# Performance work log

Hardware: AMD Instinct MI355X
Metric: run time of the kernel (lower is better)

The kernel has to match this reference:

```python
import jax, jax.numpy as jnp
import numpy as np

# Regular batched tree: BS roots, arity A, depth D (root=level 0, leaves=level D)
BS, A, D = 32, 4, 6
V, E, H = 50000, 256, 256
LEVEL_SIZES = [BS * A ** d for d in range(D + 1)]
OFFSETS = np.concatenate([[0], np.cumsum(LEVEL_SIZES)]).astype(np.int64)
TOTAL = int(OFFSETS[-1])  # 174752


def gru_cell(x, h, w_ih, w_hh, b_ih, b_hh):
    # torch nn.GRU single step, gate order (r, z, n)
    gi = x @ w_ih.T + b_ih
    gh = h @ w_hh.T + b_hh
    ir, iz, inn = jnp.split(gi, 3, axis=-1)
    hr, hz, hn = jnp.split(gh, 3, axis=-1)
    r = jax.nn.sigmoid(ir + hr)
    z = jax.nn.sigmoid(iz + hz)
    n = jnp.tanh(inn + r * hn)
    return (1.0 - z) * n + z * h


def child_attention(h_last, sent_weight, sent_bias, context_weight):
    # Reproduces hidden_per_child stacking: ch[g,c,i,:] = h_last[g,c] if c==i else 0.
    G, S, _ = h_last.shape
    eye = jnp.eye(S, dtype=h_last.dtype)
    ch = h_last[:, :, None, :] * eye[None, :, :, None]          # [G,S(c),S(i),H]
    t1 = jnp.tanh(jnp.einsum('gcih,hk->gcik', ch, sent_weight) + sent_bias[0])
    u = jnp.tanh(jnp.einsum('gcik,ko->gci', t1, context_weight))  # [G,S,S]
    w = jax.nn.softmax(u, axis=1)                                # softmax over c (the P axis)
    return jnp.einsum('gci,gcih->gih', w, ch)                    # [G,S,H]


def setup_inputs() -> dict:
    key = jax.random.key(0)
    ks = jax.random.split(key, 9)
    s = 1.0 / np.sqrt(H)
    return {
        'tokens': jax.random.randint(ks[0], (TOTAL,), 0, V, dtype=jnp.int32),
        'embedding': jax.random.normal(ks[1], (V, E), jnp.float32) * 0.1,
        'w_ih': jax.random.uniform(ks[2], (3 * H, E), jnp.float32, -s, s),
        'w_hh': jax.random.uniform(ks[3], (3 * H, H), jnp.float32, -s, s),
        'b_ih': jax.random.uniform(ks[4], (3 * H,), jnp.float32, -s, s),
        'b_hh': jax.random.uniform(ks[5], (3 * H,), jnp.float32, -s, s),
        'sent_weight': jax.random.normal(ks[6], (H, H), jnp.float32) * 0.05,
        'sent_bias': jax.random.normal(ks[7], (1, H), jnp.float32) * 0.05,
        'context_weight': jax.random.normal(ks[8], (H, 1), jnp.float32) * 0.05,
    }


def reference(tokens, embedding, w_ih, w_hh, b_ih, b_hh, sent_weight, sent_bias, context_weight):
    def tok(d):
        return tokens[int(OFFSETS[d]):int(OFFSETS[d + 1])]

    gru = lambda x, h: gru_cell(x, h, w_ih, w_hh, b_ih, b_hh)

    # leaves: no children -> zero initial hidden
    h_levels = {D: gru(embedding[tok(D)], jnp.zeros((LEVEL_SIZES[D], H), jnp.float32))}

    for d in range(D - 1, -1, -1):
        h_child = h_levels[d + 1].reshape(-1, A, H)   # [N_d, A, H]
        # duplicate index_copy in torch: only last child's hidden survives per parent
        h_last = h_child[:, A - 1, :]                 # [N_d, H]
        S = BS if d == 0 else A                       # call size: bs at root, A siblings otherwise
        groups = h_last.reshape(-1, S, H)
        chs = child_attention(groups, sent_weight, sent_bias, context_weight).reshape(-1, H)
        h_levels[d] = gru(embedding[tok(d)], chs)

    # final max over node_list: root entry has all bs rows; every other call's entry has
    # only row b = hn of the LAST sibling (duplicate valid_indices), zeros elsewhere.
    out = jnp.maximum(jnp.zeros((BS, H), jnp.float32), h_levels[0])
    for d in range(1, D + 1):
        last_sib = h_levels[d].reshape(BS, -1, A, H)[:, :, A - 1, :].max(axis=1)
        out = jnp.maximum(out, last_sib)
    return out
```

## Files before the change

kernel.cpp:

```cpp
#include <hip/hip_runtime.h>
#include <hip/hip_bf16.h>
#include <math.h>


typedef unsigned short u16;
typedef unsigned int u32;
typedef __attribute__((ext_vector_type(8))) short s8;
typedef __attribute__((ext_vector_type(4))) float f4;
#define MFMA16(a, b, c) __builtin_amdgcn_mfma_f32_16x16x32_bf16(a, b, c, 0, 0, 0)

__device__ __forceinline__ u16 f2bf(float f) {
  u32 x = __float_as_uint(f);
  return (u16)((x + 0x7fffu + ((x >> 16) & 1u)) >> 16);
}
__device__ __forceinline__ float bf2f(u16 u) { return __uint_as_float(((u32)u) << 16); }
__device__ __forceinline__ float sigmoidf_(float x) {
  return __builtin_amdgcn_rcpf(1.f + __builtin_amdgcn_exp2f(-1.4426950408889634f * x));
}
__device__ __forceinline__ float tanhf_(float x) {
  x = fminf(fmaxf(x, -15.f), 15.f);
  float t = __builtin_amdgcn_exp2f(-2.8853900817779268f * x);
  return 1.f - 2.f * t * __builtin_amdgcn_rcpf(1.f + t);
}
__device__ __forceinline__ void gload_lds16(const void* g, void* l) {
  typedef const __attribute__((address_space(1))) unsigned int* gp_t;
  typedef __attribute__((address_space(3))) unsigned int* lp_t;
  __builtin_amdgcn_global_load_lds((gp_t)g, (lp_t)l, 16, 0, 0);
}
__device__ __forceinline__ void stage_row(const float* __restrict__ emb, int tok,
                                          u16* aX, int r, int lane) {
  float4 v = ((const float4*)(emb + (size_t)tok * 256))[lane];
  uint2 val = {(u32)f2bf(v.x) | ((u32)f2bf(v.y) << 16),
               (u32)f2bf(v.z) | ((u32)f2bf(v.w) << 16)};
  *(uint2*)&aX[r * 256 + ((((lane >> 1)) ^ (r & 7)) << 3) + (lane & 1) * 4] = val;
}

__global__ void prep_pack(const float* __restrict__ wih, const float* __restrict__ whh,
                          const float* __restrict__ sw, const float* __restrict__ sb,
                          const float* __restrict__ cw,
                          u16* __restrict__ wihP, u16* __restrict__ whhPh,
                          u16* __restrict__ whhPl, u16* __restrict__ swPh,
                          float* __restrict__ u0p, int* __restrict__ outI) {
  int b = blockIdx.x, t = threadIdx.x;
  if (b == 320) {
    #pragma unroll
    for (int k = 0; k < 32; ++k) outI[k * 256 + t] = 0;
    if (t < 64) {
      float s = 0.f;
      #pragma unroll
      for (int q = 0; q < 4; ++q) { int k = t + 64 * q; s += tanhf(sb[k]) * cw[k]; }
      #pragma unroll
      for (int off = 32; off >= 1; off >>= 1) s += __shfl_xor(s, off);
      if (t == 0) u0p[0] = tanhf(s);
    }
    return;
  }
  int g = b * 256 + t;
  const float* src;
  u16* dst;
  int idx, NF, lomode, trans;
  if (g < 24576)      { idx = g;         src = wih; dst = wihP;  NF = 48; lomode = 0; trans = 1; }
  else if (g < 49152) { idx = g - 24576; src = whh; dst = whhPh; NF = 48; lomode = 0; trans = 1; }
  else if (g < 73728) { idx = g - 49152; src = whh; dst = whhPl; NF = 48; lomode = 1; trans = 1; }
  else                { idx = g - 73728; src = sw;  dst = swPh;  NF = 16; lomode = 0; trans = 0; }
  int lane = idx & 63;
  int t2 = idx >> 6;
  int nf = t2 % NF, kb = t2 / NF;
  int n = nf * 16 + (lane & 15);
  int k0 = kb * 32 + (lane >> 4) * 8;
  float v[8];
  if (trans) {
    const float4* p = (const float4*)(src + (size_t)n * 256 + k0);
    float4 a = p[0], b2 = p[1];
    v[0] = a.x; v[1] = a.y; v[2] = a.z; v[3] = a.w;
    v[4] = b2.x; v[5] = b2.y; v[6] = b2.z; v[7] = b2.w;
  } else {
    #pragma unroll
    for (int j = 0; j < 8; ++j) v[j] = src[(size_t)(k0 + j) * 256 + n];
  }
  u16 o[8];
  #pragma unroll
  for (int j = 0; j < 8; ++j) {
    u16 hi = f2bf(v[j]);
    o[j] = lomode ? f2bf(v[j] - bf2f(hi)) : hi;
  }
  u32* d = (u32*)(dst + (size_t)idx * 8);
  #pragma unroll
  for (int j = 0; j < 4; ++j) d[j] = (u32)o[2 * j] | ((u32)o[2 * j + 1] << 16);
}

__global__ __launch_bounds__(512, 2)
void levelAB_kernel(const int* __restrict__ t6, const int* __restrict__ t5,
                    const float* __restrict__ emb,
                    const u16* __restrict__ wihP, const u16* __restrict__ whhPh,
                    const u16* __restrict__ whhPl, const u16* __restrict__ swPh,
                    const float* __restrict__ bih, const float* __restrict__ bhh,
                    const float* __restrict__ sb, const float* __restrict__ cw,
                    const float* __restrict__ u0p,
                    u16* __restrict__ Hs5Hi, u16* __restrict__ Hs5Lo,
                    int* __restrict__ outI) {
  __shared__ u16 aX6[32768];
  __shared__ u16 aX5[8192];
  __shared__ u16 aH[2][8192];
  __shared__ float pm[8][32];
  __shared__ float scl[32];

  const int t = threadIdx.x;
  const int rb = blockIdx.x;
  const int lane = t & 63, w = t >> 6;
  const int asub = lane >> 4, l15 = lane & 15;
  const float LN3 = 1.0986122886681098f;

  {
    #pragma unroll
    for (int rr = 0; rr < 16; ++rr) {
      int r = 16 * w + rr;
      int tok = t6[4 * (128 * rb + r) + 3];
      stage_row(emb, tok, aX6, r, lane);
    }
    #pragma unroll
    for (int rr = 0; rr < 4; ++rr) {
      int r = 4 * w + rr;
      int tok = t5[4 * (32 * rb + r) + 3];
      stage_row(emb, tok, aX5, r, lane);
    }
  }
  __syncthreads();

  #pragma unroll 1
  for (int pass = 0; pass < 4; ++pass) {
    const int sp = pass >> 1, jc = pass & 1;
    const int cfx = 2 * w + jc;
    f4 gi[3][4];
    #pragma unroll
    for (int g = 0; g < 3; ++g)
      #pragma unroll
      for (int mf = 0; mf < 4; ++mf) gi[g][mf] = (f4){0.f, 0.f, 0.f, 0.f};
    s8 bw[2][3];
    auto LB = [&](int kb, int pb) {
      #pragma unroll
      for (int g = 0; g < 3; ++g)
        bw[pb][g] = *(const s8*)&wihP[((size_t)(kb * 48 + 16 * g + cfx) * 64 + lane) * 8];
    };
    LB(0, 0);
    #pragma unroll
    for (int kb = 0; kb < 8; ++kb) {
      const int pb = kb & 1;
      if (kb < 7) LB(kb + 1, pb ^ 1);
      s8 axh[4];
      #pragma unroll
      for (int mf = 0; mf < 4; ++mf) {
        int abase = (64 * sp + 16 * mf + l15) * 256 + (((kb * 4 + asub) ^ (l15 & 7)) << 3);
        axh[mf] = *(const s8*)&aX6[abase];
      }
      #pragma unroll
      for (int g = 0; g < 3; ++g)
        #pragma unroll
        for (int mf = 0; mf < 4; ++mf)
          gi[g][mf] = MFMA16(axh[mf], bw[pb][g], gi[g][mf]);
    }
    const int col = 16 * cfx + l15;
    const float bi0 = bih[col], bi1 = bih[256 + col], bi2 = bih[512 + col];
    const float bh0 = bhh[col], bh1 = bhh[256 + col], bh2 = bhh[512 + col];
    float cm = -1e30f;
    #pragma unroll
    for (int mf = 0; mf < 4; ++mf) {
      #pragma unroll
      for (int j = 0; j < 4; ++j) {
        float r = sigmoidf_(gi[0][mf][j] + bi0 + bh0);
        float z = sigmoidf_(gi[1][mf][j] + bi1 + bh1);
        float n = tanhf_(gi[2][mf][j] + bi2 + r * bh2);
        float h = (1.f - z) * n;
        if (j == 3) {
          int ci = 16 * sp + 4 * mf + asub;
          u16 hi = f2bf(h);
          u16 lo = f2bf(h - bf2f(hi));
          int hidx = ((col >> 3) * 32 + ci) * 8 + (col & 7);
          aH[0][hidx] = hi;
          aH[1][hidx] = lo;
        }
        cm = fmaxf(cm, h);
      }
    }
    cm = fmaxf(cm, __shfl_xor(cm, 16));
    cm = fmaxf(cm, __shfl_xor(cm, 32));
    if (asub == 0)
      atomicMax(outI + (size_t)(rb >> 3) * 256 + col, __float_as_int(cm));
  }
  __syncthreads();

  f4 sa[2][2];
  #pragma unroll
  for (int jc = 0; jc < 2; ++jc)
    #pragma unroll
    for (int mf = 0; mf < 2; ++mf) sa[jc][mf] = (f4){0.f, 0.f, 0.f, 0.f};
  {
    s8 bsw[2][2];
    auto LSW = [&](int kb, int pb) {
      #pragma unroll
      for (int jc = 0; jc < 2; ++jc)
        bsw[pb][jc] = *(const s8*)&swPh[((size_t)(kb * 16 + 2 * w + jc) * 64 + lane) * 8];
    };
    LSW(0, 0);
    #pragma unroll
    for (int kb = 0; kb < 8; ++kb) {
      const int pb = kb & 1;
      if (kb < 7) LSW(kb + 1, pb ^ 1);
      s8 ahh[2], ahl[2];
      #pragma unroll
      for (int mf = 0; mf < 2; ++mf) {
        int abase = ((kb * 4 + asub) * 32 + 16 * mf + l15) * 8;
        ahh[mf] = *(const s8*)&aH[0][abase];
        ahl[mf] = *(const s8*)&aH[1][abase];
      }
      #pragma unroll
      for (int jc = 0; jc < 2; ++jc) {
        sa[jc][0] = MFMA16(ahh[0], bsw[pb][jc], sa[jc][0]);
        sa[jc][1] = MFMA16(ahh[1], bsw[pb][jc], sa[jc][1]);
        sa[jc][0] = MFMA16(ahl[0], bsw[pb][jc], sa[jc][0]);
        sa[jc][1] = MFMA16(ahl[1], bsw[pb][jc], sa[jc][1]);
      }
    }
  }
  {
    float part[2][4] = {{0.f, 0.f, 0.f, 0.f}, {0.f, 0.f, 0.f, 0.f}};
    #pragma unroll
    for (int jc = 0; jc < 2; ++jc) {
      int k = 16 * (2 * w + jc) + l15;
      float sbk = sb[k], cwk = cw[k];
      #pragma unroll
      for (int mf = 0; mf < 2; ++mf)
        #pragma unroll
        for (int j = 0; j < 4; ++j) part[mf][j] += tanhf_(sa[jc][mf][j] + sbk) * cwk;
    }
    #pragma unroll
    for (int mf = 0; mf < 2; ++mf)
      #pragma unroll
      for (int j = 0; j < 4; ++j) {
        part[mf][j] += __shfl_xor(part[mf][j], 1);
        part[mf][j] += __shfl_xor(part[mf][j], 2);
        part[mf][j] += __shfl_xor(part[mf][j], 4);
        part[mf][j] += __shfl_xor(part[mf][j], 8);
      }
    if (l15 == 0) {
      #pragma unroll
      for (int mf = 0; mf < 2; ++mf)
        #pragma unroll
        for (int j = 0; j < 4; ++j) pm[w][16 * mf + 4 * asub + j] = part[mf][j];
    }
    __syncthreads();
    if (t < 32) {
      float v = 0.f;
      #pragma unroll
      for (int q = 0; q < 8; ++q) v += pm[q][t];
      scl[t] = sigmoidf_(tanhf_(v) - u0p[0] - LN3);
    }
    __syncthreads();
  }
  #pragma unroll 1
  for (int pass = 0; pass < 4; ++pass) {
    const int p = pass >> 1, mf = pass & 1;
    const int cf = w + 8 * p;
    f4 gi5[3], gh5[3];
    #pragma unroll
    for (int g = 0; g < 3; ++g) {
      gi5[g] = (f4){0.f, 0.f, 0.f, 0.f};
      gh5[g] = (f4){0.f, 0.f, 0.f, 0.f};
    }
    #pragma unroll
    for (int kb = 0; kb < 8; ++kb) {
      s8 bwi[3], bwh[3], bwl[3];
      #pragma unroll
      for (int g = 0; g < 3; ++g) {
        size_t bo = ((size_t)(kb * 48 + 16 * g + cf) * 64 + lane) * 8;
        bwi[g] = *(const s8*)&wihP[bo];
        bwh[g] = *(const s8*)&whhPh[bo];
        bwl[g] = *(const s8*)&whhPl[bo];
      }
      int axb = (16 * mf + l15) * 256 + (((kb * 4 + asub) ^ (l15 & 7)) << 3);
      s8 axh = *(const s8*)&aX5[axb];
      int abase = ((kb * 4 + asub) * 32 + 16 * mf + l15) * 8;
      s8 ahh = *(const s8*)&aH[0][abase];
      s8 ahl = *(const s8*)&aH[1][abase];
      #pragma unroll
      for (int g = 0; g < 3; ++g) {
        gi5[g] = MFMA16(axh, bwi[g], gi5[g]);
        gh5[g] = MFMA16(ahh, bwh[g], gh5[g]);
        gh5[g] = MFMA16(ahl, bwh[g], gh5[g]);
        gh5[g] = MFMA16(ahh, bwl[g], gh5[g]);
      }
    }
    const int col = 16 * cf + l15;
    const float bi0 = bih[col], bi1 = bih[256 + col], bi2 = bih[512 + col];
    const float bh0 = bhh[col], bh1 = bhh[256 + col], bh2 = bhh[512 + col];
    const int r0 = 16 * mf + 4 * asub;
    float cm = -1e30f;
    #pragma unroll
    for (int j = 0; j < 4; ++j) {
      const int row = r0 + j;
      const int i = 32 * rb + row;
      float sc = scl[row];
      float ir = gi5[0][j] + bi0;
      float iz = gi5[1][j] + bi1;
      float inn = gi5[2][j] + bi2;
      float g0 = bh0 + sc * gh5[0][j];
      float g1 = bh1 + sc * gh5[1][j];
      float g2 = bh2 + sc * gh5[2][j];
      int hidx = ((col >> 3) * 32 + row) * 8 + (col & 7);
      float hp = sc * (bf2f(aH[0][hidx]) + bf2f(aH[1][hidx]));
      float r = sigmoidf_(ir + g0);
      float z = sigmoidf_(iz + g1);
      float n = tanhf_(inn + r * g2);
      float h = (1.f - z) * n + z * hp;
      if (j == 3) {
        u16 hi = f2bf(h);
        u16 lo = f2bf(h - bf2f(hi));
        Hs5Hi[(size_t)(i >> 2) * 256 + col] = hi;
        Hs5Lo[(size_t)(i >> 2) * 256 + col] = lo;
      }
      cm = fmaxf(cm, h);
    }
    cm = fmaxf(cm, __shfl_xor(cm, 16));
    cm = fmaxf(cm, __shfl_xor(cm, 32));
    if (asub == 0)
      atomicMax(outI + (size_t)(rb >> 3) * 256 + col, __float_as_int(cm));
  }
}

__global__ __launch_bounds__(512, 2)
void levelB_kernel(const int* __restrict__ tokens, const float* __restrict__ emb,
                   const u16* __restrict__ wihP, const u16* __restrict__ whhPh,
                   const u16* __restrict__ whhPl, const u16* __restrict__ swPh,
                   const float* __restrict__ bih, const float* __restrict__ bhh,
                   const float* __restrict__ sb, const float* __restrict__ cw,
                   const float* __restrict__ u0p,
                   const u16* __restrict__ HpHi, const u16* __restrict__ HpLo,
                   u16* __restrict__ HoutHi, u16* __restrict__ HoutLo,
                   int* __restrict__ outI, float logSm1, int bshift) {
  __shared__ u16 aX[8192];
  __shared__ u16 aH[2][8192];
  __shared__ float pm[8][32];
  __shared__ float scl[32];

  const int t = threadIdx.x;
  const int rb = blockIdx.x >> 1, cb = blockIdx.x & 1;
  const int i0 = rb * 32;
  const int lane = t & 63, w = t >> 6;

  {
    int row = lane & 31;
    const u16* sh = HpHi + ((size_t)(i0 + row) << 8);
    const u16* sl = HpLo + ((size_t)(i0 + row) << 8);
    #pragma unroll
    for (int c = 0; c < 2; ++c) {
      int cg = w * 4 + c * 2 + (lane >> 5);
      int lb = w * 1024 + c * 512;
      gload_lds16(sh + (cg << 3), &aH[0][lb]);
      gload_lds16(sl + (cg << 3), &aH[1][lb]);
    }
  }
  {
    #pragma unroll
    for (int rr = 0; rr < 4; ++rr) {
      int r = 4 * w + rr;
      int tok = tokens[4 * (i0 + r) + 3];
      stage_row(emb, tok, aX, r, lane);
    }
  }
  __syncthreads();

  const int asub = lane >> 4, l15 = lane & 15;
  const int cfg = 8 * cb + w;

  f4 gi[3][2], gh[3][2], sa[2][2];
  #pragma unroll
  for (int g = 0; g < 3; ++g)
    #pragma unroll
    for (int mf = 0; mf < 2; ++mf) {
      gi[g][mf] = (f4){0.f, 0.f, 0.f, 0.f};
      gh[g][mf] = (f4){0.f, 0.f, 0.f, 0.f};
    }
  #pragma unroll
  for (int jc = 0; jc < 2; ++jc)
    #pragma unroll
    for (int mf = 0; mf < 2; ++mf) sa[jc][mf] = (f4){0.f, 0.f, 0.f, 0.f};

  #pragma unroll
  for (int kb = 0; kb < 8; ++kb) {
    s8 bwi[3], bwh[3], bwl[3], bsw[2];
    #pragma unroll
    for (int g = 0; g < 3; ++g) {
      size_t bo = ((size_t)(kb * 48 + 16 * g + cfg) * 64 + lane) * 8;
      bwi[g] = *(const s8*)&wihP[bo];
      bwh[g] = *(const s8*)&whhPh[bo];
      bwl[g] = *(const s8*)&whhPl[bo];
    }
    #pragma unroll
    for (int jc = 0; jc < 2; ++jc) {
      size_t so = ((size_t)(kb * 16 + 2 * w + jc) * 64 + lane) * 8;
      bsw[jc] = *(const s8*)&swPh[so];
    }
    s8 axh[2], ahh[2], ahl[2];
    #pragma unroll
    for (int mf = 0; mf < 2; ++mf) {
      int axb = (16 * mf + l15) * 256 + (((kb * 4 + asub) ^ (l15 & 7)) << 3);
      axh[mf] = *(const s8*)&aX[axb];
      int abase = ((kb * 4 + asub) * 32 + 16 * mf + l15) * 8;
      ahh[mf] = *(const s8*)&aH[0][abase];
      ahl[mf] = *(const s8*)&aH[1][abase];
    }
    #pragma unroll
    for (int g = 0; g < 3; ++g) {
      gi[g][0] = MFMA16(axh[0], bwi[g], gi[g][0]);
      gi[g][1] = MFMA16(axh[1], bwi[g], gi[g][1]);
      gh[g][0] = MFMA16(ahh[0], bwh[g], gh[g][0]);
      gh[g][1] = MFMA16(ahh[1], bwh[g], gh[g][1]);
      gh[g][0] = MFMA16(ahl[0], bwh[g], gh[g][0]);
      gh[g][1] = MFMA16(ahl[1], bwh[g], gh[g][1]);
      gh[g][0] = MFMA16(ahh[0], bwl[g], gh[g][0]);
      gh[g][1] = MFMA16(ahh[1], bwl[g], gh[g][1]);
    }
    #pragma unroll
    for (int jc = 0; jc < 2; ++jc) {
      sa[jc][0] = MFMA16(ahh[0], bsw[jc], sa[jc][0]);
      sa[jc][1] = MFMA16(ahh[1], bsw[jc], sa[jc][1]);
      sa[jc][0] = MFMA16(ahl[0], bsw[jc], sa[jc][0]);
      sa[jc][1] = MFMA16(ahl[1], bsw[jc], sa[jc][1]);
    }
  }

  {
    float part[2][4] = {{0.f, 0.f, 0.f, 0.f}, {0.f, 0.f, 0.f, 0.f}};
    #pragma unroll
    for (int jc = 0; jc < 2; ++jc) {
      int k = 16 * (2 * w + jc) + l15;
      float sbk = sb[k], cwk = cw[k];
      #pragma unroll
      for (int mf = 0; mf < 2; ++mf)
        #pragma unroll
        for (int j = 0; j < 4; ++j) part[mf][j] += tanhf_(sa[jc][mf][j] + sbk) * cwk;
    }
    #pragma unroll
    for (int mf = 0; mf < 2; ++mf)
      #pragma unroll
      for (int j = 0; j < 4; ++j) {
        part[mf][j] += __shfl_xor(part[mf][j], 1);
        part[mf][j] += __shfl_xor(part[mf][j], 2);
        part[mf][j] += __shfl_xor(part[mf][j], 4);
        part[mf][j] += __shfl_xor(part[mf][j], 8);
      }
    if (l15 == 0) {
      #pragma unroll
      for (int mf = 0; mf < 2; ++mf)
        #pragma unroll
        for (int j = 0; j < 4; ++j) pm[w][16 * mf + 4 * asub + j] = part[mf][j];
    }
    __syncthreads();
    if (t < 32) {
      float v = 0.f;
      #pragma unroll
      for (int q = 0; q < 8; ++q) v += pm[q][t];
      scl[t] = sigmoidf_(tanhf_(v) - u0p[0] - logSm1);
    }
    __syncthreads();
  }

  {
    const int col = 16 * cfg + l15;
    const float bi0 = bih[col], bi1 = bih[256 + col], bi2 = bih[512 + col];
    const float bh0 = bhh[col], bh1 = bhh[256 + col], bh2 = bhh[512 + col];
    float cmax = -1e30f;
    #pragma unroll
    for (int mf = 0; mf < 2; ++mf) {
      const int r0 = 16 * mf + 4 * asub;
      #pragma unroll
      for (int j = 0; j < 4; ++j) {
        const int row = r0 + j;
        const int i = i0 + row;
        float sc = scl[row];
        float ir = gi[0][mf][j] + bi0;
        float iz = gi[1][mf][j] + bi1;
        float inn = gi[2][mf][j] + bi2;
        float g0 = bh0 + sc * gh[0][mf][j];
        float g1 = bh1 + sc * gh[1][mf][j];
        float g2 = bh2 + sc * gh[2][mf][j];
        int hidx = ((col >> 3) * 32 + row) * 8 + (col & 7);
        float hp = sc * (bf2f(aH[0][hidx]) + bf2f(aH[1][hidx]));
        float r = sigmoidf_(ir + g0);
        float z = sigmoidf_(iz + g1);
        float n = tanhf_(inn + r * g2);
        float h = (1.f - z) * n + z * hp;
        if ((i & 3) == 3) {
          u16 hi = f2bf(h);
          u16 lo = f2bf(h - bf2f(hi));
          HoutHi[(size_t)(i >> 2) * 256 + col] = hi;
          HoutLo[(size_t)(i >> 2) * 256 + col] = lo;
        }
        cmax = fmaxf(cmax, h);
      }
    }
    cmax = fmaxf(cmax, __shfl_xor(cmax, 16));
    cmax = fmaxf(cmax, __shfl_xor(cmax, 32));
    if (asub == 0)
      atomicMax(outI + (size_t)(i0 >> bshift) * 256 + col, __float_as_int(cmax));
  }
}

struct Bregs {
  s8 wi[3], wh[3], wl[3], sw[4];
};
__device__ __forceinline__ void loadB(int kb, int cf, int wq, int lane,
                                      const u16* __restrict__ wihP,
                                      const u16* __restrict__ whhPh,
                                      const u16* __restrict__ whhPl,
                                      const u16* __restrict__ swPh, Bregs& r) {
  #pragma unroll
  for (int g = 0; g < 3; ++g) {
    size_t bo = ((size_t)(kb * 48 + 16 * g + cf) * 64 + lane) * 8;
    r.wi[g] = *(const s8*)&wihP[bo];
    r.wh[g] = *(const s8*)&whhPh[bo];
    r.wl[g] = *(const s8*)&whhPl[bo];
  }
  #pragma unroll
  for (int c = 0; c < 4; ++c) {
    size_t so = ((size_t)(kb * 16 + 4 * wq + c) * 64 + lane) * 8;
    r.sw[c] = *(const s8*)&swPh[so];
  }
}

template <bool ROOT>
__global__ __launch_bounds__(512, 2)
void tail_kernel(const int* __restrict__ tokens, const float* __restrict__ emb,
                 const u16* __restrict__ wihP, const u16* __restrict__ whhPh,
                 const u16* __restrict__ whhPl, const u16* __restrict__ swPh,
                 const float* __restrict__ bih, const float* __restrict__ bhh,
                 const float* __restrict__ sb, const float* __restrict__ cw,
                 const float* __restrict__ u0p,
                 const u16* __restrict__ HpHi, const u16* __restrict__ HpLo,
                 u16* __restrict__ HoutHi, u16* __restrict__ HoutLo,
                 int* __restrict__ outI, float logSm1, int bshift, int store_mode) {
  __shared__ u16 aX[8192];
  __shared__ u16 aH[2][8192];
  __shared__ float pm[8][32];
  __shared__ float scl[32];

  const int t = threadIdx.x;
  const int rb = blockIdx.x >> 2, cb = blockIdx.x & 3;
  const int i0 = rb * 32;
  const int lane = t & 63, w = t >> 6;

  {
    int row = lane & 31;
    const u16* sh = HpHi + ((size_t)(i0 + row) << 8);
    const u16* sl = HpLo + ((size_t)(i0 + row) << 8);
    #pragma unroll
    for (int c = 0; c < 2; ++c) {
      int cg = w * 4 + c * 2 + (lane >> 5);
      int lb = w * 1024 + c * 512;
      gload_lds16(sh + (cg << 3), &aH[0][lb]);
      gload_lds16(sl + (cg << 3), &aH[1][lb]);
    }
  }
  {
    #pragma unroll
    for (int rr = 0; rr < 4; ++rr) {
      int r = 4 * w + rr;
      int tok = tokens[ROOT ? (i0 + r) : (4 * (i0 + r) + 3)];
      stage_row(emb, tok, aX, r, lane);
    }
  }
  __syncthreads();

  const int wq = w & 3, mf = w >> 2;
  const int asub = lane >> 4;
  const int l15 = lane & 15;
  const int cf = 4 * cb + wq;

  f4 gi[3], gh[3], sa[4];
  #pragma unroll
  for (int g = 0; g < 3; ++g) { gi[g] = (f4){0.f, 0.f, 0.f, 0.f}; gh[g] = (f4){0.f, 0.f, 0.f, 0.f}; }
  #pragma unroll
  for (int c = 0; c < 4; ++c) sa[c] = (f4){0.f, 0.f, 0.f, 0.f};

  Bregs b0, b1;
  loadB(0, cf, wq, lane, wihP, whhPh, whhPl, swPh, b0);

  #pragma unroll
  for (int kb = 0; kb < 8; ++kb) {
    Bregs& cur = (kb & 1) ? b1 : b0;
    Bregs& nxt = (kb & 1) ? b0 : b1;
    if (kb < 7) loadB(kb + 1, cf, wq, lane, wihP, whhPh, whhPl, swPh, nxt);
    int axb = (16 * mf + l15) * 256 + (((kb * 4 + asub) ^ (l15 & 7)) << 3);
    s8 axh = *(const s8*)&aX[axb];
    int abase = ((kb * 4 + asub) * 32 + 16 * mf + l15) * 8;
    s8 ahh = *(const s8*)&aH[0][abase];
    s8 ahl = *(const s8*)&aH[1][abase];
    #pragma unroll
    for (int g = 0; g < 3; ++g) {
      gi[g] = MFMA16(axh, cur.wi[g], gi[g]);
      gh[g] = MFMA16(ahh, cur.wh[g], gh[g]);
      gh[g] = MFMA16(ahl, cur.wh[g], gh[g]);
      gh[g] = MFMA16(ahh, cur.wl[g], gh[g]);
    }
    #pragma unroll
    for (int c = 0; c < 4; ++c) {
      sa[c] = MFMA16(ahh, cur.sw[c], sa[c]);
      sa[c] = MFMA16(ahl, cur.sw[c], sa[c]);
    }
  }

  {
    float part[4] = {0.f, 0.f, 0.f, 0.f};
    #pragma unroll
    for (int c = 0; c < 4; ++c) {
      int k = 16 * (4 * wq + c) + l15;
      float sbk = sb[k], cwk = cw[k];
      #pragma unroll
      for (int j = 0; j < 4; ++j) part[j] += tanhf_(sa[c][j] + sbk) * cwk;
    }
    #pragma unroll
    for (int j = 0; j < 4; ++j) {
      part[j] += __shfl_xor(part[j], 1);
      part[j] += __shfl_xor(part[j], 2);
      part[j] += __shfl_xor(part[j], 4);
      part[j] += __shfl_xor(part[j], 8);
    }
    if (l15 == 0) {
      #pragma unroll
      for (int j = 0; j < 4; ++j) pm[w][16 * mf + 4 * asub + j] = part[j];
    }
    __syncthreads();
    if (t < 32) {
      int q0 = (t >> 4) * 4;
      float v = pm[q0][t] + pm[q0 + 1][t] + pm[q0 + 2][t] + pm[q0 + 3][t];
      scl[t] = sigmoidf_(tanhf_(v) - u0p[0] - logSm1);
    }
    __syncthreads();
  }

  {
    const int col = 16 * cf + l15;
    const float bi0 = bih[col], bi1 = bih[256 + col], bi2 = bih[512 + col];
    const float bh0 = bhh[col], bh1 = bhh[256 + col], bh2 = bhh[512 + col];
    const int r0 = 16 * mf + 4 * asub;
    float hmax = -1e30f;
    #pragma unroll
    for (int j = 0; j < 4; ++j) {
      const int row = r0 + j;
      const int i = i0 + row;
      float sc = scl[row];
      float ir = gi[0][j] + bi0;
      float iz = gi[1][j] + bi1;
      float inn = gi[2][j] + bi2;
      float g0 = bh0 + sc * gh[0][j];
      float g1 = bh1 + sc * gh[1][j];
      float g2 = bh2 + sc * gh[2][j];
      int hidx = ((col >> 3) * 32 + row) * 8 + (col & 7);
      float hp = sc * (bf2f(aH[0][hidx]) + bf2f(aH[1][hidx]));
      float r = sigmoidf_(ir + g0);
      float z = sigmoidf_(iz + g1);
      float n = tanhf_(inn + r * g2);
      float h = (1.f - z) * n + z * hp;
      if (store_mode == 1) {
        u16 hi = f2bf(h);
        u16 lo = f2bf(h - bf2f(hi));
        HoutHi[(size_t)i * 256 + col] = hi;
        HoutLo[(size_t)i * 256 + col] = lo;
      } else if (store_mode == 2 && ((i & 3) == 3)) {
        u16 hi = f2bf(h);
        u16 lo = f2bf(h - bf2f(hi));
        HoutHi[(size_t)(i >> 2) * 256 + col] = hi;
        HoutLo[(size_t)(i >> 2) * 256 + col] = lo;
      }
      if (bshift >= 2) {
        hmax = (j == 0) ? h : fmaxf(hmax, h);
      } else {
        atomicMax(outI + (size_t)i * 256 + col, __float_as_int(h));
      }
    }
    if (bshift >= 4) {
      hmax = fmaxf(hmax, __shfl_xor(hmax, 16));
      hmax = fmaxf(hmax, __shfl_xor(hmax, 32));
      if (asub == 0)
        atomicMax(outI + (size_t)((i0 + 16 * mf) >> bshift) * 256 + col,
                  __float_as_int(hmax));
    } else if (bshift >= 2) {
      atomicMax(outI + (size_t)((i0 + r0) >> bshift) * 256 + col, __float_as_int(hmax));
    }
  }
}

extern "C" void kernel_launch(void* const* d_in, const int* in_sizes, int n_in,
                              void* d_out, int out_size, void* d_ws, size_t ws_size,
                              hipStream_t stream) {
  const int*   tokens = (const int*)d_in[0];
  const float* emb    = (const float*)d_in[1];
  const float* wih    = (const float*)d_in[2];
  const float* whh    = (const float*)d_in[3];
  const float* bih    = (const float*)d_in[4];
  const float* bhh    = (const float*)d_in[5];
  const float* sw     = (const float*)d_in[6];
  const float* sb     = (const float*)d_in[7];
  const float* cw     = (const float*)d_in[8];

  char* ws = (char*)d_ws;
  u16* wihP  = (u16*)(ws + 0);
  u16* whhPh = (u16*)(ws + 393216);
  u16* whhPl = (u16*)(ws + 786432);
  u16* swPh  = (u16*)(ws + 1179648);
  float* u0p = (float*)(ws + 1310720);
  u16* H1Hi  = (u16*)(ws + 1310976);
  u16* H1Lo  = (u16*)(ws + 1327360);
  u16* Hs5Hi = (u16*)(ws + 9961472);
  u16* Hs5Lo = (u16*)(ws + 11010048);
  u16* Hs4Hi = (u16*)(ws + 12058624);
  u16* Hs4Lo = (u16*)(ws + 12320768);
  u16* Hs3Hi = (u16*)(ws + 12582912);
  u16* Hs3Lo = (u16*)(ws + 12648448);
  u16* Hs2Hi = (u16*)(ws + 12713984);
  u16* Hs2Lo = (u16*)(ws + 12730368);

  int* outI = (int*)d_out;
  prep_pack<<<321, 256, 0, stream>>>(wih, whh, sw, sb, cw,
                                     wihP, whhPh, whhPl, swPh, u0p, outI);

  const float LN3  = 1.0986122886681098f;
  const float LN31 = 3.4339872044851463f;

  levelAB_kernel<<<256, 512, 0, stream>>>(
      tokens + 43680, tokens + 10912, emb, wihP, whhPh, whhPl, swPh,
      bih, bhh, sb, cw, u0p, Hs5Hi, Hs5Lo, outI);
  levelB_kernel<<<128, 512, 0, stream>>>(
      tokens + 2720, emb, wihP, whhPh, whhPl, swPh, bih, bhh, sb, cw, u0p,
      Hs5Hi, Hs5Lo, Hs4Hi, Hs4Lo, outI, LN3, 6);
  tail_kernel<false><<<64, 512, 0, stream>>>(
      tokens + 672, emb, wihP, whhPh, whhPl, swPh, bih, bhh, sb, cw, u0p,
      Hs4Hi, Hs4Lo, Hs3Hi, Hs3Lo, outI, LN3, 4, 2);
  tail_kernel<false><<<16, 512, 0, stream>>>(
      tokens + 160, emb, wihP, whhPh, whhPl, swPh, bih, bhh, sb, cw, u0p,
      Hs3Hi, Hs3Lo, Hs2Hi, Hs2Lo, outI, LN3, 2, 2);
  tail_kernel<false><<<4, 512, 0, stream>>>(
      tokens + 32, emb, wihP, whhPh, whhPl, swPh, bih, bhh, sb, cw, u0p,
      Hs2Hi, Hs2Lo, H1Hi, H1Lo, outI, LN3, 0, 1);
  tail_kernel<true><<<4, 512, 0, stream>>>(
      tokens + 0, emb, wihP, whhPh, whhPl, swPh, bih, bhh, sb, cw, u0p,
      H1Hi, H1Lo, nullptr, nullptr, outI, LN31, 0, 0);
}
```

Baseline: 119.9 us.

## Fuse tree levels 6-3 into one kernel and levels 2-0 into a tail kernel

Extends the leaf kernel so each block also computes levels 4 and 3 of its own subtree in LDS, reusing the aX6 buffer for the intermediate hidden states. Only the level-3 last-sibling states go to global memory. A new 8-block tail kernel then runs levels 2, 1 and 0 in LDS. This replaces six launches with two and removes the global round trips between levels. In exchange, the small levels run with little parallelism inside each block (16-row MFMA tiles, many barriers), and the tail runs on only 8 blocks.

```diff
diff --git a/kernel.cpp b/kernel.cpp
--- a/kernel.cpp
+++ b/kernel.cpp
@@ -21,11 +21,6 @@
   x = fminf(fmaxf(x, -15.f), 15.f);
   float t = __builtin_amdgcn_exp2f(-2.8853900817779268f * x);
   return 1.f - 2.f * t * __builtin_amdgcn_rcpf(1.f + t);
-}
-__device__ __forceinline__ void gload_lds16(const void* g, void* l) {
-  typedef const __attribute__((address_space(1))) unsigned int* gp_t;
-  typedef __attribute__((address_space(3))) unsigned int* lp_t;
-  __builtin_amdgcn_global_load_lds((gp_t)g, (lp_t)l, 16, 0, 0);
 }
 __device__ __forceinline__ void stage_row(const float* __restrict__ emb, int tok,
                                           u16* aX, int r, int lane) {
@@ -89,40 +84,188 @@
   for (int j = 0; j < 4; ++j) d[j] = (u32)o[2 * j] | ((u32)o[2 * j + 1] << 16);
 }
 
+__device__ __forceinline__ void level16(
+    const u16* __restrict__ aXp, const u16* __restrict__ aHh,
+    const u16* __restrict__ aHl,
+    const u16* __restrict__ wihP, const u16* __restrict__ whhPh,
+    const u16* __restrict__ whhPl, const u16* __restrict__ swPh,
+    const float* __restrict__ bih, const float* __restrict__ bhh,
+    const float* __restrict__ sb, const float* __restrict__ cw, float u0v,
+    float logSm1, int nvalid, u16* outHh, u16* outHl, int outMode,
+    u16* __restrict__ gHi, u16* __restrict__ gLo, int gB, int doG,
+    int* __restrict__ outI, int mode, int batchBase,
+    float (*pm)[32], float* scl, int t) {
+  const int lane = t & 63, w = t >> 6;
+  const int asub = lane >> 4, l15 = lane & 15;
+  f4 sa0 = (f4){0.f, 0.f, 0.f, 0.f}, sa1 = (f4){0.f, 0.f, 0.f, 0.f};
+  #pragma unroll
+  for (int kb = 0; kb < 8; ++kb) {
+    s8 b0 = *(const s8*)&swPh[((size_t)(kb * 16 + 2 * w) * 64 + lane) * 8];
+    s8 b1 = *(const s8*)&swPh[((size_t)(kb * 16 + 2 * w + 1) * 64 + lane) * 8];
+    int ab = ((kb * 4 + asub) * 16 + l15) * 8;
+    s8 ahh = *(const s8*)&aHh[ab];
+    s8 ahl = *(const s8*)&aHl[ab];
+    sa0 = MFMA16(ahh, b0, sa0); sa0 = MFMA16(ahl, b0, sa0);
+    sa1 = MFMA16(ahh, b1, sa1); sa1 = MFMA16(ahl, b1, sa1);
+  }
+  {
+    float part[4] = {0.f, 0.f, 0.f, 0.f};
+    #pragma unroll
+    for (int jc = 0; jc < 2; ++jc) {
+      int k = 16 * (2 * w + jc) + l15;
+      float sbk = sb[k], cwk = cw[k];
+      #pragma unroll
+      for (int j = 0; j < 4; ++j)
+        part[j] += tanhf_((jc ? sa1[j] : sa0[j]) + sbk) * cwk;
+    }
+    #pragma unroll
+    for (int j = 0; j < 4; ++j) {
+      part[j] += __shfl_xor(part[j], 1);
+      part[j] += __shfl_xor(part[j], 2);
+      part[j] += __shfl_xor(part[j], 4);
+      part[j] += __shfl_xor(part[j], 8);
+    }
+    if (l15 == 0) {
+      #pragma unroll
+      for (int j = 0; j < 4; ++j) pm[w][4 * asub + j] = part[j];
+    }
+    __syncthreads();
+    if (t < 16) {
+      float v = 0.f;
+      #pragma unroll
+      for (int q = 0; q < 8; ++q) v += pm[q][t];
+      scl[t] = sigmoidf_(tanhf_(v) - u0v - logSm1);
+    }
+    __syncthreads();
+  }
+  #pragma unroll 1
+  for (int p = 0; p < 2; ++p) {
+    const int cf = w + 8 * p;
+    f4 gi5[3], gh5[3];
+    #pragma unroll
+    for (int g = 0; g < 3; ++g) {
+      gi5[g] = (f4){0.f, 0.f, 0.f, 0.f};
+      gh5[g] = (f4){0.f, 0.f, 0.f, 0.f};
+    }
+    #pragma unroll
+    for (int kb = 0; kb < 8; ++kb) {
+      s8 bwi[3], bwh[3], bwl[3];
+      #pragma unroll
+      for (int g = 0; g < 3; ++g) {
+        size_t bo = ((size_t)(kb * 48 + 16 * g + cf) * 64 + lane) * 8;
+        bwi[g] = *(const s8*)&wihP[bo];
+        bwh[g] = *(const s8*)&whhPh[bo];
+        bwl[g] = *(const s8*)&whhPl[bo];
+      }
+      int axb = l15 * 256 + (((kb * 4 + asub) ^ (l15 & 7)) << 3);
+      s8 axh = *(const s8*)&aXp[axb];
+      int ab = ((kb * 4 + asub) * 16 + l15) * 8;
+      s8 ahh = *(const s8*)&aHh[ab];
+      s8 ahl = *(const s8*)&aHl[ab];
+      #pragma unroll
+      for (int g = 0; g < 3; ++g) {
+        gi5[g] = MFMA16(axh, bwi[g], gi5[g]);
+        gh5[g] = MFMA16(ahh, bwh[g], gh5[g]);
+        gh5[g] = MFMA16(ahl, bwh[g], gh5[g]);
+        gh5[g] = MFMA16(ahh, bwl[g], gh5[g]);
+      }
+    }
+    const int col = 16 * cf + l15;
+    const float bi0 = bih[col], bi1 = bih[256 + col], bi2 = bih[512 + col];
+    const float bh0 = bhh[col], bh1 = bhh[256 + col], bh2 = bhh[512 + col];
+    float cm = -1e30f;
+    #pragma unroll
+    for (int j = 0; j < 4; ++j) {
+      const int row = 4 * asub + j;
+      const int valid = row < nvalid;
+      float sc = scl[row];
+      float ir = gi5[0][j] + bi0;
+      float iz = gi5[1][j] + bi1;
+      float inn = gi5[2][j] + bi2;
+      float g0 = bh0 + sc * gh5[0][j];
+      float g1 = bh1 + sc * gh5[1][j];
+      float g2 = bh2 + sc * gh5[2][j];
+      int hix = ((col >> 3) * 16 + row) * 8 + (col & 7);
+      float hp = sc * (bf2f(aHh[hix]) + bf2f(aHl[hix]));
+      float r = sigmoidf_(ir + g0);
+      float z = sigmoidf_(iz + g1);
+      float n = tanhf_(inn + r * g2);
+      float h = (1.f - z) * n + z * hp;
+      u16 hi = f2bf(h);
+      u16 lo = f2bf(h - bf2f(hi));
+      if (outMode == 1 && j == 3 && valid) {
+        int ho = ((col >> 3) * 16 + asub) * 8 + (col & 7);
+        outHh[ho] = hi; outHl[ho] = lo;
+      } else if (outMode == 2 && valid) {
+        outHh[hix] = hi; outHl[hix] = lo;
+      }
+      if (doG && valid) {
+        int gidx = gB + row;
+        if ((gidx & 3) == 3) {
+          gHi[(size_t)(gidx >> 2) * 256 + col] = hi;
+          gLo[(size_t)(gidx >> 2) * 256 + col] = lo;
+        }
+      }
+      if (mode == 2) {
+        if (valid)
+          atomicMax(outI + (size_t)(batchBase + row) * 256 + col, __float_as_int(h));
+      } else if (valid) {
+        cm = fmaxf(cm, h);
+      }
+    }
+    if (mode == 1) {
+      atomicMax(outI + (size_t)(batchBase + asub) * 256 + col, __float_as_int(cm));
+    } else if (mode == 0) {
+      cm = fmaxf(cm, __shfl_xor(cm, 16));
+      cm = fmaxf(cm, __shfl_xor(cm, 32));
+      if (asub == 0)
+        atomicMax(outI + (size_t)batchBase * 256 + col, __float_as_int(cm));
+    }
+  }
+}
+
 __global__ __launch_bounds__(512, 2)
-void levelAB_kernel(const int* __restrict__ t6, const int* __restrict__ t5,
-                    const float* __restrict__ emb,
-                    const u16* __restrict__ wihP, const u16* __restrict__ whhPh,
-                    const u16* __restrict__ whhPl, const u16* __restrict__ swPh,
-                    const float* __restrict__ bih, const float* __restrict__ bhh,
-                    const float* __restrict__ sb, const float* __restrict__ cw,
-                    const float* __restrict__ u0p,
-                    u16* __restrict__ Hs5Hi, u16* __restrict__ Hs5Lo,
-                    int* __restrict__ outI) {
+void levelABCD_kernel(const int* __restrict__ t6, const int* __restrict__ t5,
+                      const int* __restrict__ t4, const int* __restrict__ t3,
+                      const float* __restrict__ emb,
+                      const u16* __restrict__ wihP, const u16* __restrict__ whhPh,
+                      const u16* __restrict__ whhPl, const u16* __restrict__ swPh,
+                      const float* __restrict__ bih, const float* __restrict__ bhh,
+                      const float* __restrict__ sb, const float* __restrict__ cw,
+                      const float* __restrict__ u0p,
+                      u16* __restrict__ Hs3Hi, u16* __restrict__ Hs3Lo,
+                      int* __restrict__ outI) {
   __shared__ u16 aX6[32768];
   __shared__ u16 aX5[8192];
   __shared__ u16 aH[2][8192];
   __shared__ float pm[8][32];
   __shared__ float scl[32];
 
+  u16* aH4h = aX6;
+  u16* aH4l = aX6 + 4096;
+  u16* aX4  = aX6 + 8192;
+  u16* aH3h = aX6 + 12288;
+  u16* aH3l = aX6 + 16384;
+  u16* aX3  = aX6 + 20480;
+
   const int t = threadIdx.x;
   const int rb = blockIdx.x;
   const int lane = t & 63, w = t >> 6;
   const int asub = lane >> 4, l15 = lane & 15;
   const float LN3 = 1.0986122886681098f;
+  const float u0v = u0p[0];
+  const int batch = rb >> 3;
 
   {
     #pragma unroll
     for (int rr = 0; rr < 16; ++rr) {
       int r = 16 * w + rr;
-      int tok = t6[4 * (128 * rb + r) + 3];
-      stage_row(emb, tok, aX6, r, lane);
+      stage_row(emb, t6[4 * (128 * rb + r) + 3], aX6, r, lane);
     }
     #pragma unroll
     for (int rr = 0; rr < 4; ++rr) {
       int r = 4 * w + rr;
-      int tok = t5[4 * (32 * rb + r) + 3];
-      stage_row(emb, tok, aX5, r, lane);
+      stage_row(emb, t5[4 * (32 * rb + r) + 3], aX5, r, lane);
     }
   }
   __syncthreads();
@@ -150,8 +293,8 @@
       s8 axh[4];
       #pragma unroll
       for (int mf = 0; mf < 4; ++mf) {
-        int abase = (64 * sp + 16 * mf + l15) * 256 + (((kb * 4 + asub) ^ (l15 & 7)) << 3);
-        axh[mf] = *(const s8*)&aX6[abase];
+        int ab = (64 * sp + 16 * mf + l15) * 256 + (((kb * 4 + asub) ^ (l15 & 7)) << 3);
+        axh[mf] = *(const s8*)&aX6[ab];
       }
       #pragma unroll
       for (int g = 0; g < 3; ++g)
@@ -185,9 +328,12 @@
     cm = fmaxf(cm, __shfl_xor(cm, 16));
     cm = fmaxf(cm, __shfl_xor(cm, 32));
     if (asub == 0)
-      atomicMax(outI + (size_t)(rb >> 3) * 256 + col, __float_as_int(cm));
-  }
-  __syncthreads();
+      atomicMax(outI + (size_t)batch * 256 + col, __float_as_int(cm));
+  }
+  __syncthreads();
+
+  if (w < 8) stage_row(emb, t4[4 * (8 * rb + w) + 3], aX4, w, lane);
+  if (w < 2) stage_row(emb, t3[4 * (2 * rb + w) + 3], aX3, w, lane);
 
   f4 sa[2][2];
   #pragma unroll
@@ -209,9 +355,9 @@
       s8 ahh[2], ahl[2];
       #pragma unroll
       for (int mf = 0; mf < 2; ++mf) {
-        int abase = ((kb * 4 + asub) * 32 + 16 * mf + l15) * 8;
-        ahh[mf] = *(const s8*)&aH[0][abase];
-        ahl[mf] = *(const s8*)&aH[1][abase];
+        int ab = ((kb * 4 + asub) * 32 + 16 * mf + l15) * 8;
+        ahh[mf] = *(const s8*)&aH[0][ab];
+        ahl[mf] = *(const s8*)&aH[1][ab];
       }
       #pragma unroll
       for (int jc = 0; jc < 2; ++jc) {
@@ -253,7 +399,7 @@
       float v = 0.f;
       #pragma unroll
       for (int q = 0; q < 8; ++q) v += pm[q][t];
-      scl[t] = sigmoidf_(tanhf_(v) - u0p[0] - LN3);
+      scl[t] = sigmoidf_(tanhf_(v) - u0v - LN3);
     }
     __syncthreads();
   }
@@ -279,9 +425,9 @@
       }
       int axb = (16 * mf + l15) * 256 + (((kb * 4 + asub) ^ (l15 & 7)) << 3);
       s8 axh = *(const s8*)&aX5[axb];
-      int abase = ((kb * 4 + asub) * 32 + 16 * mf + l15) * 8;
-      s8 ahh = *(const s8*)&aH[0][abase];
-      s8 ahl = *(const s8*)&aH[1][abase];
+      int ab = ((kb * 4 + asub) * 32 + 16 * mf + l15) * 8;
+      s8 ahh = *(const s8*)&aH[0][ab];
+      s8 ahl = *(const s8*)&aH[1][ab];
       #pragma unroll
       for (int g = 0; g < 3; ++g) {
         gi5[g] = MFMA16(axh, bwi[g], gi5[g]);
@@ -298,7 +444,6 @@
     #pragma unroll
     for (int j = 0; j < 4; ++j) {
       const int row = r0 + j;
-      const int i = 32 * rb + row;
       float sc = scl[row];
       float ir = gi5[0][j] + bi0;
       float iz = gi5[1][j] + bi1;
@@ -315,379 +460,77 @@
       if (j == 3) {
         u16 hi = f2bf(h);
         u16 lo = f2bf(h - bf2f(hi));
-        Hs5Hi[(size_t)(i >> 2) * 256 + col] = hi;
-        Hs5Lo[(size_t)(i >> 2) * 256 + col] = lo;
+        int ho = ((col >> 3) * 16 + 4 * mf + asub) * 8 + (col & 7);
+        aH4h[ho] = hi; aH4l[ho] = lo;
       }
       cm = fmaxf(cm, h);
     }
     cm = fmaxf(cm, __shfl_xor(cm, 16));
     cm = fmaxf(cm, __shfl_xor(cm, 32));
     if (asub == 0)
-      atomicMax(outI + (size_t)(rb >> 3) * 256 + col, __float_as_int(cm));
-  }
+      atomicMax(outI + (size_t)batch * 256 + col, __float_as_int(cm));
+  }
+  __syncthreads();
+
+  level16(aX4, aH4h, aH4l, wihP, whhPh, whhPl, swPh, bih, bhh, sb, cw, u0v,
+          LN3, 8, aH3h, aH3l, 1, nullptr, nullptr, 0, 0,
+          outI, 0, batch, pm, scl, t);
+  __syncthreads();
+
+  level16(aX3, aH3h, aH3l, wihP, whhPh, whhPl, swPh, bih, bhh, sb, cw, u0v,
+          LN3, 2, nullptr, nullptr, 0, Hs3Hi, Hs3Lo, 2 * rb, 1,
+          outI, 0, batch, pm, scl, t);
 }
 
 __global__ __launch_bounds__(512, 2)
-void levelB_kernel(const int* __restrict__ tokens, const float* __restrict__ emb,
-                   const u16* __restrict__ wihP, const u16* __restrict__ whhPh,
-                   const u16* __restrict__ whhPl, const u16* __restrict__ swPh,
-                   const float* __restrict__ bih, const float* __restrict__ bhh,
-                   const float* __restrict__ sb, const float* __restrict__ cw,
-                   const float* __restrict__ u0p,
-                   const u16* __restrict__ HpHi, const u16* __restrict__ HpLo,
-                   u16* __restrict__ HoutHi, u16* __restrict__ HoutLo,
-                   int* __restrict__ outI, float logSm1, int bshift) {
-  __shared__ u16 aX[8192];
-  __shared__ u16 aH[2][8192];
+void tailF_kernel(const int* __restrict__ t2, const int* __restrict__ t1,
+                  const int* __restrict__ t0, const float* __restrict__ emb,
+                  const u16* __restrict__ wihP, const u16* __restrict__ whhPh,
+                  const u16* __restrict__ whhPl, const u16* __restrict__ swPh,
+                  const float* __restrict__ bih, const float* __restrict__ bhh,
+                  const float* __restrict__ sb, const float* __restrict__ cw,
+                  const float* __restrict__ u0p,
+                  const u16* __restrict__ Hs3Hi, const u16* __restrict__ Hs3Lo,
+                  int* __restrict__ outI) {
+  __shared__ u16 aX2[4096], aH2h[4096], aH2l[4096];
+  __shared__ u16 aX1[4096], aH1h[4096], aH1l[4096];
+  __shared__ u16 aX0[4096], aH0h[4096], aH0l[4096];
   __shared__ float pm[8][32];
   __shared__ float scl[32];
 
   const int t = threadIdx.x;
-  const int rb = blockIdx.x >> 1, cb = blockIdx.x & 1;
-  const int i0 = rb * 32;
+  const int b = blockIdx.x;
   const int lane = t & 63, w = t >> 6;
+  const float LN3 = 1.0986122886681098f;
+  const float LN31 = 3.4339872044851463f;
+  const float u0v = u0p[0];
 
   {
-    int row = lane & 31;
-    const u16* sh = HpHi + ((size_t)(i0 + row) << 8);
-    const u16* sl = HpLo + ((size_t)(i0 + row) << 8);
-    #pragma unroll
-    for (int c = 0; c < 2; ++c) {
-      int cg = w * 4 + c * 2 + (lane >> 5);
-      int lb = w * 1024 + c * 512;
-      gload_lds16(sh + (cg << 3), &aH[0][lb]);
-      gload_lds16(sl + (cg << 3), &aH[1][lb]);
-    }
-  }
-  {
-    #pragma unroll
-    for (int rr = 0; rr < 4; ++rr) {
-      int r = 4 * w + rr;
-      int tok = tokens[4 * (i0 + r) + 3];
-      stage_row(emb, tok, aX, r, lane);
-    }
-  }
-  __syncthreads();
-
-  const int asub = lane >> 4, l15 = lane & 15;
-  const int cfg = 8 * cb + w;
-
-  f4 gi[3][2], gh[3][2], sa[2][2];
-  #pragma unroll
-  for (int g = 0; g < 3; ++g)
-    #pragma unroll
-    for (int mf = 0; mf < 2; ++mf) {
-      gi[g][mf] = (f4){0.f, 0.f, 0.f, 0.f};
-      gh[g][mf] = (f4){0.f, 0.f, 0.f, 0.f};
-    }
-  #pragma unroll
-  for (int jc = 0; jc < 2; ++jc)
-    #pragma unroll
-    for (int mf = 0; mf < 2; ++mf) sa[jc][mf] = (f4){0.f, 0.f, 0.f, 0.f};
-
-  #pragma unroll
-  for (int kb = 0; kb < 8; ++kb) {
-    s8 bwi[3], bwh[3], bwl[3], bsw[2];
-    #pragma unroll
-    for (int g = 0; g < 3; ++g) {
-      size_t bo = ((size_t)(kb * 48 + 16 * g + cfg) * 64 + lane) * 8;
-      bwi[g] = *(const s8*)&wihP[bo];
-      bwh[g] = *(const s8*)&whhPh[bo];
-      bwl[g] = *(const s8*)&whhPl[bo];
-    }
-    #pragma unroll
-    for (int jc = 0; jc < 2; ++jc) {
-      size_t so = ((size_t)(kb * 16 + 2 * w + jc) * 64 + lane) * 8;
-      bsw[jc] = *(const s8*)&swPh[so];
-    }
-    s8 axh[2], ahh[2], ahl[2];
-    #pragma unroll
-    for (int mf = 0; mf < 2; ++mf) {
-      int axb = (16 * mf + l15) * 256 + (((kb * 4 + asub) ^ (l15 & 7)) << 3);
-      axh[mf] = *(const s8*)&aX[axb];
-      int abase = ((kb * 4 + asub) * 32 + 16 * mf + l15) * 8;
-      ahh[mf] = *(const s8*)&aH[0][abase];
-      ahl[mf] = *(const s8*)&aH[1][abase];
-    }
-    #pragma unroll
-    for (int g = 0; g < 3; ++g) {
-      gi[g][0] = MFMA16(axh[0], bwi[g], gi[g][0]);
-      gi[g][1] = MFMA16(axh[1], bwi[g], gi[g][1]);
-      gh[g][0] = MFMA16(ahh[0], bwh[g], gh[g][0]);
-      gh[g][1] = MFMA16(ahh[1], bwh[g], gh[g][1]);
-      gh[g][0] = MFMA16(ahl[0], bwh[g], gh[g][0]);
-      gh[g][1] = MFMA16(ahl[1], bwh[g], gh[g][1]);
-      gh[g][0] = MFMA16(ahh[0], bwl[g], gh[g][0]);
-      gh[g][1] = MFMA16(ahh[1], bwl[g], gh[g][1]);
-    }
-    #pragma unroll
-    for (int jc = 0; jc < 2; ++jc) {
-      sa[jc][0] = MFMA16(ahh[0], bsw[jc], sa[jc][0]);
-      sa[jc][1] = MFMA16(ahh[1], bsw[jc], sa[jc][1]);
-      sa[jc][0] = MFMA16(ahl[0], bsw[jc], sa[jc][0]);
-      sa[jc][1] = MFMA16(ahl[1], bsw[jc], sa[jc][1]);
-    }
-  }
-
-  {
-    float part[2][4] = {{0.f, 0.f, 0.f, 0.f}, {0.f, 0.f, 0.f, 0.f}};
-    #pragma unroll
-    for (int jc = 0; jc < 2; ++jc) {
-      int k = 16 * (2 * w + jc) + l15;
-      float sbk = sb[k], cwk = cw[k];
-      #pragma unroll
-      for (int mf = 0; mf < 2; ++mf)
-        #pragma unroll
-        for (int j = 0; j < 4; ++j) part[mf][j] += tanhf_(sa[jc][mf][j] + sbk) * cwk;
-    }
-    #pragma unroll
-    for (int mf = 0; mf < 2; ++mf)
-      #pragma unroll
-      for (int j = 0; j < 4; ++j) {
-        part[mf][j] += __shfl_xor(part[mf][j], 1);
-        part[mf][j] += __shfl_xor(part[mf][j], 2);
-        part[mf][j] += __shfl_xor(part[mf][j], 4);
-        part[mf][j] += __shfl_xor(part[mf][j], 8);
-      }
-    if (l15 == 0) {
-      #pragma unroll
-      for (int mf = 0; mf < 2; ++mf)
-        #pragma unroll
-        for (int j = 0; j < 4; ++j) pm[w][16 * mf + 4 * asub + j] = part[mf][j];
-    }
-    __syncthreads();
-    if (t < 32) {
-      float v = 0.f;
-      #pragma unroll
-      for (int q = 0; q < 8; ++q) v += pm[q][t];
-      scl[t] = sigmoidf_(tanhf_(v) - u0p[0] - logSm1);
-    }
-    __syncthreads();
-  }
-
-  {
-    const int col = 16 * cfg + l15;
-    const float bi0 = bih[col], bi1 = bih[256 + col], bi2 = bih[512 + col];
-    const float bh0 = bhh[col], bh1 = bhh[256 + col], bh2 = bhh[512 + col];
-    float cmax = -1e30f;
-    #pragma unroll
-    for (int mf = 0; mf < 2; ++mf) {
-      const int r0 = 16 * mf + 4 * asub;
-      #pragma unroll
-      for (int j = 0; j < 4; ++j) {
-        const int row = r0 + j;
-        const int i = i0 + row;
-        float sc = scl[row];
-        float ir = gi[0][mf][j] + bi0;
-        float iz = gi[1][mf][j] + bi1;
-        float inn = gi[2][mf][j] + bi2;
-        float g0 = bh0 + sc * gh[0][mf][j];
-        float g1 = bh1 + sc * gh[1][mf][j];
-        float g2 = bh2 + sc * gh[2][mf][j];
-        int hidx = ((col >> 3) * 32 + row) * 8 + (col & 7);
-        float hp = sc * (bf2f(aH[0][hidx]) + bf2f(aH[1][hidx]));
-        float r = sigmoidf_(ir + g0);
-        float z = sigmoidf_(iz + g1);
-        float n = tanhf_(inn + r * g2);
-        float h = (1.f - z) * n + z * hp;
-        if ((i & 3) == 3) {
-          u16 hi = f2bf(h);
-          u16 lo = f2bf(h - bf2f(hi));
-          HoutHi[(size_t)(i >> 2) * 256 + col] = hi;
-          HoutLo[(size_t)(i >> 2) * 256 + col] = lo;
-        }
-        cmax = fmaxf(cmax, h);
-      }
-    }
-    cmax = fmaxf(cmax, __shfl_xor(cmax, 16));
-    cmax = fmaxf(cmax, __shfl_xor(cmax, 32));
-    if (asub == 0)
-      atomicMax(outI + (size_t)(i0 >> bshift) * 256 + col, __float_as_int(cmax));
-  }
-}
-
-struct Bregs {
-  s8 wi[3], wh[3], wl[3], sw[4];
-};
-__device__ __forceinline__ void loadB(int kb, int cf, int wq, int lane,
-                                      const u16* __restrict__ wihP,
-                                      const u16* __restrict__ whhPh,
-                                      const u16* __restrict__ whhPl,
-                                      const u16* __restrict__ swPh, Bregs& r) {
-  #pragma unroll
-  for (int g = 0; g < 3; ++g) {
-    size_t bo = ((size_t)(kb * 48 + 16 * g + cf) * 64 + lane) * 8;
-    r.wi[g] = *(const s8*)&wihP[bo];
-    r.wh[g] = *(const s8*)&whhPh[bo];
-    r.wl[g] = *(const s8*)&whhPl[bo];
-  }
-  #pragma unroll
-  for (int c = 0; c < 4; ++c) {
-    size_t so = ((size_t)(kb * 16 + 4 * wq + c) * 64 + lane) * 8;
-    r.sw[c] = *(const s8*)&swPh[so];
-  }
-}
-
-template <bool ROOT>
-__global__ __launch_bounds__(512, 2)
-void tail_kernel(const int* __restrict__ tokens, const float* __restrict__ emb,
-                 const u16* __restrict__ wihP, const u16* __restrict__ whhPh,
-                 const u16* __restrict__ whhPl, const u16* __restrict__ swPh,
-                 const float* __restrict__ bih, const float* __restrict__ bhh,
-                 const float* __restrict__ sb, const float* __restrict__ cw,
-                 const float* __restrict__ u0p,
-                 const u16* __restrict__ HpHi, const u16* __restrict__ HpLo,
-                 u16* __restrict__ HoutHi, u16* __restrict__ HoutLo,
-                 int* __restrict__ outI, float logSm1, int bshift, int store_mode) {
-  __shared__ u16 aX[8192];
-  __shared__ u16 aH[2][8192];
-  __shared__ float pm[8][32];
-  __shared__ float scl[32];
-
-  const int t = threadIdx.x;
-  const int rb = blockIdx.x >> 2, cb = blockIdx.x & 3;
-  const int i0 = rb * 32;
-  const int lane = t & 63, w = t >> 6;
-
-  {
-    int row = lane & 31;
-    const u16* sh = HpHi + ((size_t)(i0 + row) << 8);
-    const u16* sl = HpLo + ((size_t)(i0 + row) << 8);
-    #pragma unroll
-    for (int c = 0; c < 2; ++c) {
-      int cg = w * 4 + c * 2 + (lane >> 5);
-      int lb = w * 1024 + c * 512;
-      gload_lds16(sh + (cg << 3), &aH[0][lb]);
-      gload_lds16(sl + (cg << 3), &aH[1][lb]);
-    }
-  }
-  {
-    #pragma unroll
-    for (int rr = 0; rr < 4; ++rr) {
-      int r = 4 * w + rr;
-      int tok = tokens[ROOT ? (i0 + r) : (4 * (i0 + r) + 3)];
-      stage_row(emb, tok, aX, r, lane);
-    }
-  }
-  __syncthreads();
-
-  const int wq = w & 3, mf = w >> 2;
-  const int asub = lane >> 4;
-  const int l15 = lane & 15;
-  const int cf = 4 * cb + wq;
-
-  f4 gi[3], gh[3], sa[4];
-  #pragma unroll
-  for (int g = 0; g < 3; ++g) { gi[g] = (f4){0.f, 0.f, 0.f, 0.f}; gh[g] = (f4){0.f, 0.f, 0.f, 0.f}; }
-  #pragma unroll
-  for (int c = 0; c < 4; ++c) sa[c] = (f4){0.f, 0.f, 0.f, 0.f};
-
-  Bregs b0, b1;
-  loadB(0, cf, wq, lane, wihP, whhPh, whhPl, swPh, b0);
-
-  #pragma unroll
-  for (int kb = 0; kb < 8; ++kb) {
-    Bregs& cur = (kb & 1) ? b1 : b0;
-    Bregs& nxt = (kb & 1) ? b0 : b1;
-    if (kb < 7) loadB(kb + 1, cf, wq, lane, wihP, whhPh, whhPl, swPh, nxt);
-    int axb = (16 * mf + l15) * 256 + (((kb * 4 + asub) ^ (l15 & 7)) << 3);
-    s8 axh = *(const s8*)&aX[axb];
-    int abase = ((kb * 4 + asub) * 32 + 16 * mf + l15) * 8;
-    s8 ahh = *(const s8*)&aH[0][abase];
-    s8 ahl = *(const s8*)&aH[1][abase];
-    #pragma unroll
-    for (int g = 0; g < 3; ++g) {
-      gi[g] = MFMA16(axh, cur.wi[g], gi[g]);
-      gh[g] = MFMA16(ahh, cur.wh[g], gh[g]);
-      gh[g] = MFMA16(ahl, cur.wh[g], gh[g]);
-      gh[g] = MFMA16(ahh, cur.wl[g], gh[g]);
-    }
-    #pragma unroll
-    for (int c = 0; c < 4; ++c) {
-      sa[c] = MFMA16(ahh, cur.sw[c], sa[c]);
-      sa[c] = MFMA16(ahl, cur.sw[c], sa[c]);
-    }
-  }
-
-  {
-    float part[4] = {0.f, 0.f, 0.f, 0.f};
-    #pragma unroll
-    for (int c = 0; c < 4; ++c) {
-      int k = 16 * (4 * wq + c) + l15;
-      float sbk = sb[k], cwk = cw[k];
-      #pragma unroll
-      for (int j = 0; j < 4; ++j) part[j] += tanhf_(sa[c][j] + sbk) * cwk;
-    }
-    #pragma unroll
-    for (int j = 0; j < 4; ++j) {
-      part[j] += __shfl_xor(part[j], 1);
-      part[j] += __shfl_xor(part[j], 2);
-      part[j] += __shfl_xor(part[j], 4);
-      part[j] += __shfl_xor(part[j], 8);
-    }
-    if (l15 == 0) {
-      #pragma unroll
-      for (int j = 0; j < 4; ++j) pm[w][16 * mf + 4 * asub + j] = part[j];
-    }
-    __syncthreads();
-    if (t < 32) {
-      int q0 = (t >> 4) * 4;
-      float v = pm[q0][t] + pm[q0 + 1][t] + pm[q0 + 2][t] + pm[q0 + 3][t];
-      scl[t] = sigmoidf_(tanhf_(v) - u0p[0] - logSm1);
-    }
-    __syncthreads();
-  }
-
-  {
-    const int col = 16 * cf + l15;
-    const float bi0 = bih[col], bi1 = bih[256 + col], bi2 = bih[512 + col];
-    const float bh0 = bhh[col], bh1 = bhh[256 + col], bh2 = bhh[512 + col];
-    const int r0 = 16 * mf + 4 * asub;
-    float hmax = -1e30f;
-    #pragma unroll
-    for (int j = 0; j < 4; ++j) {
-      const int row = r0 + j;
-      const int i = i0 + row;
-      float sc = scl[row];
-      float ir = gi[0][j] + bi0;
-      float iz = gi[1][j] + bi1;
-      float inn = gi[2][j] + bi2;
-      float g0 = bh0 + sc * gh[0][j];
-      float g1 = bh1 + sc * gh[1][j];
-      float g2 = bh2 + sc * gh[2][j];
-      int hidx = ((col >> 3) * 32 + row) * 8 + (col & 7);
-      float hp = sc * (bf2f(aH[0][hidx]) + bf2f(aH[1][hidx]));
-      float r = sigmoidf_(ir + g0);
-      float z = sigmoidf_(iz + g1);
-      float n = tanhf_(inn + r * g2);
-      float h = (1.f - z) * n + z * hp;
-      if (store_mode == 1) {
-        u16 hi = f2bf(h);
-        u16 lo = f2bf(h - bf2f(hi));
-        HoutHi[(size_t)i * 256 + col] = hi;
-        HoutLo[(size_t)i * 256 + col] = lo;
-      } else if (store_mode == 2 && ((i & 3) == 3)) {
-        u16 hi = f2bf(h);
-        u16 lo = f2bf(h - bf2f(hi));
-        HoutHi[(size_t)(i >> 2) * 256 + col] = hi;
-        HoutLo[(size_t)(i >> 2) * 256 + col] = lo;
-      }
-      if (bshift >= 2) {
-        hmax = (j == 0) ? h : fmaxf(hmax, h);
-      } else {
-        atomicMax(outI + (size_t)i * 256 + col, __float_as_int(h));
-      }
-    }
-    if (bshift >= 4) {
-      hmax = fmaxf(hmax, __shfl_xor(hmax, 16));
-      hmax = fmaxf(hmax, __shfl_xor(hmax, 32));
-      if (asub == 0)
-        atomicMax(outI + (size_t)((i0 + 16 * mf) >> bshift) * 256 + col,
-                  __float_as_int(hmax));
-    } else if (bshift >= 2) {
-      atomicMax(outI + (size_t)((i0 + r0) >> bshift) * 256 + col, __float_as_int(hmax));
-    }
-  }
+    int row = t & 15, kg = t >> 4;
+    uint4 vh = *(const uint4*)&Hs3Hi[(size_t)(16 * b + row) * 256 + kg * 8];
+    uint4 vl = *(const uint4*)&Hs3Lo[(size_t)(16 * b + row) * 256 + kg * 8];
+    *(uint4*)&aH2h[(kg * 16 + row) * 8] = vh;
+    *(uint4*)&aH2l[(kg * 16 + row) * 8] = vl;
+    stage_row(emb, t2[4 * (16 * b + w) + 3], aX2, w, lane);
+    stage_row(emb, t2[4 * (16 * b + w + 8) + 3], aX2, w + 8, lane);
+    if (w < 4) stage_row(emb, t1[4 * (4 * b + w) + 3], aX1, w, lane);
+    if (w < 4) stage_row(emb, t0[4 * b + w], aX0, w, lane);
+  }
+  __syncthreads();
+
+  level16(aX2, aH2h, aH2l, wihP, whhPh, whhPl, swPh, bih, bhh, sb, cw, u0v,
+          LN3, 16, aH1h, aH1l, 1, nullptr, nullptr, 0, 0,
+          outI, 1, 4 * b, pm, scl, t);
+  __syncthreads();
+
+  level16(aX1, aH1h, aH1l, wihP, whhPh, whhPl, swPh, bih, bhh, sb, cw, u0v,
+          LN3, 4, aH0h, aH0l, 2, nullptr, nullptr, 0, 0,
+          outI, 2, 4 * b, pm, scl, t);
+  __syncthreads();
+
+  level16(aX0, aH0h, aH0l, wihP, whhPh, whhPl, swPh, bih, bhh, sb, cw, u0v,
+          LN31, 4, nullptr, nullptr, 0, nullptr, nullptr, 0, 0,
+          outI, 2, 4 * b, pm, scl, t);
 }
 
 extern "C" void kernel_launch(void* const* d_in, const int* in_sizes, int n_in,
@@ -709,40 +552,18 @@
   u16* whhPl = (u16*)(ws + 786432);
   u16* swPh  = (u16*)(ws + 1179648);
   float* u0p = (float*)(ws + 1310720);
-  u16* H1Hi  = (u16*)(ws + 1310976);
-  u16* H1Lo  = (u16*)(ws + 1327360);
-  u16* Hs5Hi = (u16*)(ws + 9961472);
-  u16* Hs5Lo = (u16*)(ws + 11010048);
-  u16* Hs4Hi = (u16*)(ws + 12058624);
-  u16* Hs4Lo = (u16*)(ws + 12320768);
-  u16* Hs3Hi = (u16*)(ws + 12582912);
-  u16* Hs3Lo = (u16*)(ws + 12648448);
-  u16* Hs2Hi = (u16*)(ws + 12713984);
-  u16* Hs2Lo = (u16*)(ws + 12730368);
+  u16* Hs3Hi = (u16*)(ws + 1310976);
+  u16* Hs3Lo = (u16*)(ws + 1376512);
 
   int* outI = (int*)d_out;
   prep_pack<<<321, 256, 0, stream>>>(wih, whh, sw, sb, cw,
                                      wihP, whhPh, whhPl, swPh, u0p, outI);
 
-  const float LN3  = 1.0986122886681098f;
-  const float LN31 = 3.4339872044851463f;
-
-  levelAB_kernel<<<256, 512, 0, stream>>>(
-      tokens + 43680, tokens + 10912, emb, wihP, whhPh, whhPl, swPh,
-      bih, bhh, sb, cw, u0p, Hs5Hi, Hs5Lo, outI);
-  levelB_kernel<<<128, 512, 0, stream>>>(
-      tokens + 2720, emb, wihP, whhPh, whhPl, swPh, bih, bhh, sb, cw, u0p,
-      Hs5Hi, Hs5Lo, Hs4Hi, Hs4Lo, outI, LN3, 6);
-  tail_kernel<false><<<64, 512, 0, stream>>>(
-      tokens + 672, emb, wihP, whhPh, whhPl, swPh, bih, bhh, sb, cw, u0p,
-      Hs4Hi, Hs4Lo, Hs3Hi, Hs3Lo, outI, LN3, 4, 2);
-  tail_kernel<false><<<16, 512, 0, stream>>>(
-      tokens + 160, emb, wihP, whhPh, whhPl, swPh, bih, bhh, sb, cw, u0p,
-      Hs3Hi, Hs3Lo, Hs2Hi, Hs2Lo, outI, LN3, 2, 2);
-  tail_kernel<false><<<4, 512, 0, stream>>>(
-      tokens + 32, emb, wihP, whhPh, whhPl, swPh, bih, bhh, sb, cw, u0p,
-      Hs2Hi, Hs2Lo, H1Hi, H1Lo, outI, LN3, 0, 1);
-  tail_kernel<true><<<4, 512, 0, stream>>>(
-      tokens + 0, emb, wihP, whhPh, whhPl, swPh, bih, bhh, sb, cw, u0p,
-      H1Hi, H1Lo, nullptr, nullptr, outI, LN31, 0, 0);
-}
+  levelABCD_kernel<<<256, 512, 0, stream>>>(
+      tokens + 43680, tokens + 10912, tokens + 2720, tokens + 672, emb,
+      wihP, whhPh, whhPl, swPh, bih, bhh, sb, cw, u0p, Hs3Hi, Hs3Lo, outI);
+
+  tailF_kernel<<<8, 512, 0, stream>>>(
+      tokens + 160, tokens + 32, tokens, emb,
+      wihP, whhPh, whhPl, swPh, bih, bhh, sb, cw, u0p, Hs3Hi, Hs3Lo, outI);
+}
```

Result: slower. 127.7 us (+6.5%).
